# Performance work log

Hardware: AMD Instinct MI355X
Metric: run time of the kernel (lower is better)

Reference implementation:

```python
import jax, jax.numpy as jnp
import numpy as np

N, E, C, D, A, F_, H, RNF = 20000, 200000, 14, 3, 16, 128, 128, 128
CONSTANT = 1.0
LN_EPS = 1e-5


def _pool_matrix(n_channel, dtype):
    ones = np.ones((n_channel, n_channel))
    mats = []
    for i in range(n_channel):
        ws = n_channel - i
        mats.append((np.triu(ones) - np.triu(ones, k=ws)) / ws)
    return jnp.asarray(np.stack(mats), dtype)  # [C, C, C]


def _scatter_mean(src, idx, n):
    s = jax.ops.segment_sum(src, idx, num_segments=n)
    cnt = jax.ops.segment_sum(jnp.ones((src.shape[0],), src.dtype), idx, num_segments=n)
    return s / jnp.maximum(cnt, 1.0).reshape((n,) + (1,) * (src.ndim - 1))


def setup_inputs() -> dict:
    key = jax.random.key(0)
    ks = jax.random.split(key, 24)
    h = jax.random.normal(ks[0], (N, F_), jnp.float32)
    x = jax.random.normal(ks[1], (N, C, D), jnp.float32)
    channel_attr = jax.random.normal(ks[2], (N, C, A), jnp.float32)
    cw = jax.random.uniform(ks[3], (N, C), jnp.float32)
    cw = cw * (jax.random.uniform(ks[4], (N, C)) > 0.3)  # some padded channels
    cw = cw.at[:, 0].set(jax.random.uniform(ks[5], (N,)) + 0.1)  # >=1 valid channel
    row = jax.random.randint(ks[6], (E,), 0, N, dtype=jnp.int32)
    col = jax.random.randint(ks[7], (E,), 0, N, dtype=jnp.int32)

    def lin(k, din, dout):
        return 0.02 * jax.random.normal(k, (din, dout), jnp.float32), jnp.zeros((dout,), jnp.float32)

    rad_w, rad_b = lin(ks[8], A * A, RNF)
    e_w1, e_b1 = lin(ks[9], 2 * F_ + RNF, H)
    e_w2, e_b2 = lin(ks[10], H, H)
    att_w, att_b = lin(ks[11], H, 1)
    c_w1, c_b1 = lin(ks[12], H, H)
    c_w2, c_b2 = lin(ks[13], H, C)
    n_w1, n_b1 = lin(ks[14], F_ + H, H)
    n_w2, n_b2 = lin(ks[15], H, F_)
    ln_g = jnp.ones((F_,), jnp.float32)
    ln_b = jnp.zeros((F_,), jnp.float32)
    return dict(h=h, x=x, channel_attr=channel_attr, channel_weights=cw, row=row, col=col,
                rad_w=rad_w, rad_b=rad_b, e_w1=e_w1, e_b1=e_b1, e_w2=e_w2, e_b2=e_b2,
                att_w=att_w, att_b=att_b, c_w1=c_w1, c_b1=c_b1, c_w2=c_w2, c_b2=c_b2,
                n_w1=n_w1, n_b1=n_b1, n_w2=n_w2, n_b2=n_b2, ln_g=ln_g, ln_b=ln_b)


def reference(h, x, channel_attr, channel_weights, row, col,
              rad_w, rad_b, e_w1, e_b1, e_w2, e_b2, att_w, att_b,
              c_w1, c_b1, c_w2, c_b2, n_w1, n_b1, n_w2, n_b2, ln_g, ln_b):
    silu = jax.nn.silu
    n_nodes = h.shape[0]

    # ---- coord2radial (NUM_SEG = 1) ----
    # pairwise channel distances per edge: [E, C, C]
    coord_msg = jnp.linalg.norm(x[row][:, :, None, :] - x[col][:, None, :, :], axis=-1)
    coord_msg = coord_msg * (channel_weights[row][:, :, None] * channel_weights[col][:, None, :])
    # attr^T @ msg @ attr -> [E, A, A] -> [E, A*A]
    radial = jnp.einsum('eca,ecd,edb->eab', channel_attr[row], coord_msg, channel_attr[col])
    radial = radial.reshape(radial.shape[0], -1)
    radial_norm = jnp.linalg.norm(radial, axis=-1, keepdims=True) + CONSTANT
    radial = (radial @ rad_w + rad_b) / radial_norm

    channel_mask = (channel_weights != 0).astype(x.dtype)  # [N, C]
    channel_sum = jnp.sum(channel_weights != 0, axis=-1).astype(jnp.int32)  # [N]
    pooled_col = (x[col] * channel_mask[col][:, :, None]).sum(1) / channel_sum[col].astype(x.dtype)[:, None]
    coord_diff = x[row] - pooled_col[:, None, :]  # [E, C, 3]

    # ---- edge MLP + attention gate ----
    ef = silu(jnp.concatenate([h[row], h[col], radial], axis=-1) @ e_w1 + e_b1)
    ef = silu(ef @ e_w2 + e_b2)
    ef = ef * jax.nn.sigmoid(ef @ att_w + att_b)  # att_mlp active (hidden_nf == input_nf)

    # ---- RollerPooling on coord_mlp output ----
    cm = silu(ef @ c_w1 + c_b1) @ c_w2 + c_b2  # [E, C]
    pool_mat = _pool_matrix(C, ef.dtype)[channel_sum[row] - 1]  # [E, C, C]
    pooled = jnp.einsum('eij,ej->ei', pool_mat, cm)  # [E, C]
    trans = coord_diff * pooled[:, :, None]  # [E, C, 3]

    x_new = x + _scatter_mean(trans, row, n_nodes)
    agg = _scatter_mean(ef, col, n_nodes)

    nh = silu(jnp.concatenate([h, agg], axis=-1) @ n_w1 + n_b1) @ n_w2 + n_b2
    hr = h + nh
    mu = hr.mean(-1, keepdims=True)
    var = ((hr - mu) ** 2).mean(-1, keepdims=True)
    h_new = (hr - mu) * jax.lax.rsqrt(var + LN_EPS) * ln_g + ln_b
    return h_new, x_new
```

## Files before the change

kernel.cpp:

```cpp
#include <hip/hip_runtime.h>
#include <hip/hip_bf16.h>


#define TE 16
#define TM 64
#define TN 16
#define PAD 36

typedef __attribute__((ext_vector_type(8))) short bf16x8;
typedef __attribute__((ext_vector_type(4))) float f32x4;

__device__ __forceinline__ float siluf(float v) { return v / (1.f + __expf(-v)); }
__device__ __forceinline__ float sigmf(float v) { return 1.f / (1.f + __expf(-v)); }
__device__ __forceinline__ short f2bs(float f) {
  union { __hip_bfloat16 b; short s; } u;
  u.b = __float2bfloat16(f);
  return u.s;
}
__device__ __forceinline__ __hip_bfloat162 mk_bf162(float v0, float v1) {
  __hip_bfloat162 r;
  r.x = __float2bfloat16(v0);
  r.y = __float2bfloat16(v1);
  return r;
}

__global__ __launch_bounds__(256) void k_pack(
    const float* __restrict__ h, const float* __restrict__ x,
    const float* __restrict__ attr, const float* __restrict__ cw,
    const float* __restrict__ rad_w, const float* __restrict__ e_w1,
    const float* __restrict__ e_w2, const float* __restrict__ c_w1,
    const float* __restrict__ n_w1, const float* __restrict__ n_w2,
    const float* __restrict__ c_w2,
    __hip_bfloat16* __restrict__ wz_rad, __hip_bfloat16* __restrict__ wz_e1,
    __hip_bfloat16* __restrict__ wz_e2, __hip_bfloat16* __restrict__ wz_c1,
    __hip_bfloat16* __restrict__ wz_n1, __hip_bfloat16* __restrict__ wz_n2,
    __hip_bfloat16* __restrict__ wz_c2,
    __hip_bfloat16* __restrict__ attrS, __hip_bfloat16* __restrict__ hb,
    float* __restrict__ pooled_x, int* __restrict__ chsum, int Nn) {
  int idx = blockIdx.x * 256 + threadIdx.x;
  if (idx < 165888) {
    int i = idx;
    if (i >= 163840) {
      int base = i - 163840;
      int k = base >> 4, n = base & 15;
      wz_c2[(size_t)(k >> 5) * 512 + n * 32 + (k & 31)] =
          (n < 14) ? __float2bfloat16(c_w2[k * 14 + n]) : __float2bfloat16(0.f);
      return;
    }
    const float* W;
    __hip_bfloat16* O;
    int base;
    if (i < 32768) { W = rad_w; O = wz_rad; base = i; }
    else if (i < 81920) { W = e_w1; O = wz_e1; base = i - 32768; }
    else if (i < 98304) { W = e_w2; O = wz_e2; base = i - 81920; }
    else if (i < 114688) { W = c_w1; O = wz_c1; base = i - 98304; }
    else if (i < 147456) { W = n_w1; O = wz_n1; base = i - 114688; }
    else { W = n_w2; O = wz_n2; base = i - 147456; }
    int k = base >> 7, n = base & 127;
    O[(size_t)((k >> 5) * 128 + n) * 32 + (k & 31)] = __float2bfloat16(W[base]);
    return;
  }
  idx -= 165888;
  int na = Nn * 256, nh = Nn * 128;
  if (idx < na) {
    int n = idx >> 8, r = idx & 255, i2 = r >> 4, a = r & 15;
    float v = 0.f;
    if (i2 < 14) v = attr[(size_t)n * 224 + i2 * 16 + a] * cw[(size_t)n * 14 + i2];
    attrS[(size_t)n * 256 + a * 16 + i2] = __float2bfloat16(v);
    return;
  }
  idx -= na;
  if (idx < nh) {
    hb[idx] = __float2bfloat16(h[idx]);
    return;
  }
  idx -= nh;
  if (idx >= Nn) return;
  int n = idx;
  int cnt = 0;
  float sx = 0.f, sy = 0.f, sz = 0.f;
#pragma unroll
  for (int c = 0; c < 14; c++) {
    float w = cw[n * 14 + c];
    if (w != 0.f) {
      cnt++;
      sx += x[n * 42 + c * 3 + 0];
      sy += x[n * 42 + c * 3 + 1];
      sz += x[n * 42 + c * 3 + 2];
    }
  }
  chsum[n] = cnt;
  float inv = 1.f / (float)(cnt > 0 ? cnt : 1);
  pooled_x[n * 3 + 0] = sx * inv;
  pooled_x[n * 3 + 1] = sy * inv;
  pooled_x[n * 3 + 2] = sz * inv;
}

__global__ __launch_bounds__(256) void k_rad(
    const float* __restrict__ x, const __hip_bfloat16* __restrict__ attrS,
    const int* __restrict__ row, const int* __restrict__ col,
    const __hip_bfloat16* __restrict__ wz_rad, const float* __restrict__ rad_b,
    unsigned* __restrict__ cnt_row, unsigned* __restrict__ cnt_col,
    __hip_bfloat16* __restrict__ radf, int Ee) {
  __shared__ __hip_bfloat16 sW[8][16][PAD];
  __shared__ float s_rn[TE];

  const int t = threadIdx.x;
  const int e0 = blockIdx.x * TE;
  const int ne = min(TE, Ee - e0);

  if (t < ne) {
    atomicAdd(&cnt_row[row[e0 + t]], 1u);
    atomicAdd(&cnt_col[col[e0 + t]], 1u);
  }

  const int lane = t & 63, wave = t >> 6, quad = lane >> 4, mr = lane & 15;
  const int n0 = wave * 32;
  f32x4 zacc = {0.f, 0.f, 0.f, 0.f};
  const bf16x8 zero8 = {0, 0, 0, 0, 0, 0, 0, 0};

  float xr0v[4], xr1v[4], xr2v[4], xc0v[4], xc1v[4], xc2v[4];
  bf16x8 bCv[4], aRv[4];
#pragma unroll
  for (int p = 0; p < 4; p++) {
    const int e = wave * 4 + p;
    const int ge = e0 + min(e, ne - 1);
    const int re = row[ge], ce = col[ge];
    const int mrc = min(mr, 13);
    const float* xp = x + (size_t)re * 42 + mrc * 3;
    xr0v[p] = xp[0]; xr1v[p] = xp[1]; xr2v[p] = xp[2];
    const float* xq = x + (size_t)ce * 42 + mrc * 3;
    xc0v[p] = xq[0]; xc1v[p] = xq[1]; xc2v[p] = xq[2];
    bCv[p] = zero8; aRv[p] = zero8;
    if (quad < 2) {
      bCv[p] = *(const bf16x8*)&attrS[(size_t)ce * 256 + mr * 16 + quad * 8];
      aRv[p] = *(const bf16x8*)&attrS[(size_t)re * 256 + mr * 16 + quad * 8];
    }
  }

#pragma unroll
  for (int p = 0; p < 4; p++) {
    const int e = wave * 4 + p;
    const float xr0 = xr0v[p], xr1 = xr1v[p], xr2 = xr2v[p];
    const float xc0 = xc0v[p], xc1 = xc1v[p], xc2 = xc2v[p];
    bf16x8 aX = zero8, bX = zero8;
    if (quad == 0) {
      aX[0] = f2bs(xc0); aX[1] = f2bs(xc1); aX[2] = f2bs(xc2);
      bX[0] = f2bs(xr0); bX[1] = f2bs(xr1); bX[2] = f2bs(xr2);
    }
    f32x4 G = __builtin_amdgcn_mfma_f32_16x16x32_bf16(aX, bX, zacc, 0, 0, 0);
    const float nr = xr0 * xr0 + xr1 * xr1 + xr2 * xr2;
    const float nc = xc0 * xc0 + xc1 * xc1 + xc2 * xc2;
    float dD[4];
#pragma unroll
    for (int r = 0; r < 4; r++) {
      float ncj = __shfl(nc, quad * 4 + r);
      dD[r] = sqrtf(fmaxf(ncj + nr - 2.f * G[r], 0.f));
    }
    bf16x8 aD;
#pragma unroll
    for (int jj = 0; jj < 8; jj++) {
      const int qs = (quad * 2 + (jj >> 2)) & 3;
      float dv = __shfl(dD[jj & 3], (qs << 4) | mr);
      if (quad >= 2) dv = 0.f;
      aD[jj] = f2bs(dv);
    }
    f32x4 m1 = __builtin_amdgcn_mfma_f32_16x16x32_bf16(aD, bCv[p], zacc, 0, 0, 0);
    bf16x8 bM;
#pragma unroll
    for (int jj = 0; jj < 8; jj++) {
      const int qs = (quad * 2 + (jj >> 2)) & 3;
      float mv = __shfl(m1[jj & 3], (qs << 4) | mr);
      if (quad >= 2) mv = 0.f;
      bM[jj] = f2bs(mv);
    }
    f32x4 rd = __builtin_amdgcn_mfma_f32_16x16x32_bf16(aRv[p], bM, zacc, 0, 0, 0);
    float ss = rd[0] * rd[0] + rd[1] * rd[1] + rd[2] * rd[2] + rd[3] * rd[3];
    ss += __shfl_xor(ss, 32); ss += __shfl_xor(ss, 16); ss += __shfl_xor(ss, 8);
    ss += __shfl_xor(ss, 4);  ss += __shfl_xor(ss, 2);  ss += __shfl_xor(ss, 1);
    if (lane == 0) s_rn[e] = sqrtf(ss) + 1.0f;
#pragma unroll
    for (int r = 0; r < 4; r++) {
      const int aa = quad * 4 + r;
      sW[aa >> 1][e][((aa & 1) << 4) | mr] = __float2bfloat16(rd[r]);
    }
  }
  __syncthreads();

  {
    f32x4 acc0 = zacc, acc1 = zacc;
#pragma unroll
    for (int kb = 0; kb < 8; kb++) {
      bf16x8 a = *(const bf16x8*)&sW[kb][mr][quad * 8];
      const __hip_bfloat16* wp = wz_rad + ((size_t)(kb * 128 + n0 + mr) * 32 + quad * 8);
      bf16x8 b0 = *(const bf16x8*)wp;
      bf16x8 b1 = *(const bf16x8*)(wp + 16 * 32);
      acc0 = __builtin_amdgcn_mfma_f32_16x16x32_bf16(a, b0, acc0, 0, 0, 0);
      acc1 = __builtin_amdgcn_mfma_f32_16x16x32_bf16(a, b1, acc1, 0, 0, 0);
    }
    float bias0 = rad_b[n0 + mr], bias1 = rad_b[n0 + 16 + mr];
#pragma unroll
    for (int r = 0; r < 4; r++) {
      int e = quad * 4 + r;
      if (e < ne) {
        float inv = 1.f / s_rn[e];
        size_t base = (size_t)(e0 + e) * 128;
        radf[base + n0 + mr]      = __float2bfloat16((acc0[r] + bias0) * inv);
        radf[base + n0 + 16 + mr] = __float2bfloat16((acc1[r] + bias1) * inv);
      }
    }
  }
}

__global__ __launch_bounds__(256, 3) void k_mlp(
    const __hip_bfloat16* __restrict__ hb, const __hip_bfloat16* __restrict__ radf,
    const float* __restrict__ x, const float* __restrict__ pooled_x,
    const int* __restrict__ row, const int* __restrict__ col,
    const int* __restrict__ chsum,
    const __hip_bfloat16* __restrict__ wz_e1, const float* __restrict__ e_b1,
    const __hip_bfloat16* __restrict__ wz_e2, const float* __restrict__ e_b2,
    const float* __restrict__ att_w, const float* __restrict__ att_b,
    const __hip_bfloat16* __restrict__ wz_c1, const float* __restrict__ c_b1,
    const __hip_bfloat16* __restrict__ wz_c2, const float* __restrict__ c_b2,
    __hip_bfloat162* __restrict__ x_acc, __hip_bfloat162* __restrict__ agg,
    int Ee) {
  __shared__ __hip_bfloat16 S[12][TM][32];
  __shared__ float s_att[TM];
  __shared__ float s_red[4][TM];
  __shared__ int s_row[TM], s_col[TM], s_cs[TM];
  float* s_cm   = (float*)&S[0][0][0];
  float* s_pool = (float*)&S[1][0][0];

  const int t = threadIdx.x;
  const int e0 = blockIdx.x * TM;
  const int ne = min(TM, Ee - e0);

  if (t < TM) {
    int ge = e0 + min(t, ne - 1);
    int r = row[ge];
    s_row[t] = r;
    s_col[t] = col[ge];
    s_cs[t] = chsum[r];
  }
  __syncthreads();

  {
    const int m = t >> 2, part = t & 3;
    const int pc = ((part ^ ((m >> 1) & 3)) << 3);
    const __hip_bfloat16* hr = hb + (size_t)s_row[m] * 128 + part * 8;
    const __hip_bfloat16* hc = hb + (size_t)s_col[m] * 128 + part * 8;
    const __hip_bfloat16* rf = radf + (size_t)(e0 + min(m, ne - 1)) * 128 + part * 8;
#pragma unroll
    for (int kb = 0; kb < 4; kb++) {
      *(int4*)&S[kb][m][pc]     = *(const int4*)&hr[kb * 32];
      *(int4*)&S[4 + kb][m][pc] = *(const int4*)&hc[kb * 32];
      *(int4*)&S[8 + kb][m][pc] = *(const int4*)&rf[kb * 32];
    }
  }
  __syncthreads();

  const int lane = t & 63, wave = t >> 6, quad = lane >> 4, mr = lane & 15;
  const int n0 = wave * 32;
  const int acol = ((quad ^ ((mr >> 1) & 3)) << 3);
  const f32x4 zacc = {0.f, 0.f, 0.f, 0.f};

  f32x4 s1a0[4], s1a1[4];
#pragma unroll
  for (int mf = 0; mf < 4; mf++) { s1a0[mf] = zacc; s1a1[mf] = zacc; }
#pragma unroll
  for (int kb = 0; kb < 12; kb++) {
    const __hip_bfloat16* wp = wz_e1 + ((size_t)(kb * 128 + n0 + mr) * 32 + quad * 8);
    bf16x8 b0 = *(const bf16x8*)wp;
    bf16x8 b1 = *(const bf16x8*)(wp + 16 * 32);
#pragma unroll
    for (int mf = 0; mf < 4; mf++) {
      bf16x8 a = *(const bf16x8*)&S[kb][mf * 16 + mr][acol];
      s1a0[mf] = __builtin_amdgcn_mfma_f32_16x16x32_bf16(a, b0, s1a0[mf], 0, 0, 0);
      s1a1[mf] = __builtin_amdgcn_mfma_f32_16x16x32_bf16(a, b1, s1a1[mf], 0, 0, 0);
    }
  }
  __syncthreads();
  {
    float bias0 = e_b1[n0 + mr], bias1 = e_b1[n0 + 16 + mr];
#pragma unroll
    for (int mf = 0; mf < 4; mf++)
#pragma unroll
      for (int r = 0; r < 4; r++) {
        int e = mf * 16 + quad * 4 + r;
        int es = (e >> 1) & 3;
        int c0 = (((mr >> 3) ^ es) << 3) | (mr & 7);
        int c1 = (((2 | (mr >> 3)) ^ es) << 3) | (mr & 7);
        S[wave][e][c0] = __float2bfloat16(siluf(s1a0[mf][r] + bias0));
        S[wave][e][c1] = __float2bfloat16(siluf(s1a1[mf][r] + bias1));
      }
  }
  __syncthreads();

  const float aw0 = att_w[n0 + mr], aw1 = att_w[n0 + 16 + mr];
  {
    f32x4 a0[4], a1[4];
#pragma unroll
    for (int mf = 0; mf < 4; mf++) { a0[mf] = zacc; a1[mf] = zacc; }
#pragma unroll
    for (int kb = 0; kb < 4; kb++) {
      const __hip_bfloat16* wp = wz_e2 + ((size_t)(kb * 128 + n0 + mr) * 32 + quad * 8);
      bf16x8 b0 = *(const bf16x8*)wp;
      bf16x8 b1 = *(const bf16x8*)(wp + 16 * 32);
#pragma unroll
      for (int mf = 0; mf < 4; mf++) {
        bf16x8 a = *(const bf16x8*)&S[kb][mf * 16 + mr][acol];
        a0[mf] = __builtin_amdgcn_mfma_f32_16x16x32_bf16(a, b0, a0[mf], 0, 0, 0);
        a1[mf] = __builtin_amdgcn_mfma_f32_16x16x32_bf16(a, b1, a1[mf], 0, 0, 0);
      }
    }
    float bias0 = e_b2[n0 + mr], bias1 = e_b2[n0 + 16 + mr];
    float part[4][4];
#pragma unroll
    for (int mf = 0; mf < 4; mf++)
#pragma unroll
      for (int r = 0; r < 4; r++) {
        int e = mf * 16 + quad * 4 + r;
        int es = (e >> 1) & 3;
        int c0 = (((mr >> 3) ^ es) << 3) | (mr & 7);
        int c1 = (((2 | (mr >> 3)) ^ es) << 3) | (mr & 7);
        float v0 = siluf(a0[mf][r] + bias0);
        float v1 = siluf(a1[mf][r] + bias1);
        S[4 + wave][e][c0] = __float2bfloat16(v0);
        S[4 + wave][e][c1] = __float2bfloat16(v1);
        part[mf][r] = v0 * aw0 + v1 * aw1;
      }
#pragma unroll
    for (int msk = 1; msk < 16; msk <<= 1)
#pragma unroll
      for (int mf = 0; mf < 4; mf++)
#pragma unroll
        for (int r = 0; r < 4; r++) part[mf][r] += __shfl_xor(part[mf][r], msk);
    if (mr == 0) {
#pragma unroll
      for (int mf = 0; mf < 4; mf++)
#pragma unroll
        for (int r = 0; r < 4; r++)
          s_red[wave][mf * 16 + quad * 4 + r] = part[mf][r];
    }
  }
  __syncthreads();
  if (t < TM) {
    float s = s_red[0][t] + s_red[1][t] + s_red[2][t] + s_red[3][t];
    s_att[t] = sigmf(s + att_b[0]);
  }
  __syncthreads();

  {
    f32x4 a0[4], a1[4];
#pragma unroll
    for (int mf = 0; mf < 4; mf++) { a0[mf] = zacc; a1[mf] = zacc; }
#pragma unroll
    for (int kb = 0; kb < 4; kb++) {
      const __hip_bfloat16* wp = wz_c1 + ((size_t)(kb * 128 + n0 + mr) * 32 + quad * 8);
      bf16x8 b0 = *(const bf16x8*)wp;
      bf16x8 b1 = *(const bf16x8*)(wp + 16 * 32);
#pragma unroll
      for (int mf = 0; mf < 4; mf++) {
        bf16x8 a = *(const bf16x8*)&S[4 + kb][mf * 16 + mr][acol];
        a0[mf] = __builtin_amdgcn_mfma_f32_16x16x32_bf16(a, b0, a0[mf], 0, 0, 0);
        a1[mf] = __builtin_amdgcn_mfma_f32_16x16x32_bf16(a, b1, a1[mf], 0, 0, 0);
      }
    }
    float bias0 = c_b1[n0 + mr], bias1 = c_b1[n0 + 16 + mr];
#pragma unroll
    for (int mf = 0; mf < 4; mf++)
#pragma unroll
      for (int r = 0; r < 4; r++) {
        int e = mf * 16 + quad * 4 + r;
        int es = (e >> 1) & 3;
        int c0 = (((mr >> 3) ^ es) << 3) | (mr & 7);
        int c1 = (((2 | (mr >> 3)) ^ es) << 3) | (mr & 7);
        float av = s_att[e];
        S[8 + wave][e][c0] = __float2bfloat16(siluf(av * a0[mf][r] + bias0));
        S[8 + wave][e][c1] = __float2bfloat16(siluf(av * a1[mf][r] + bias1));
      }
  }
  __syncthreads();

  {
    f32x4 acc = zacc;
#pragma unroll
    for (int kb = 0; kb < 4; kb++) {
      bf16x8 a = *(const bf16x8*)&S[8 + kb][wave * 16 + mr][acol];
      bf16x8 b = *(const bf16x8*)(wz_c2 + ((size_t)(kb * 16 + mr) * 32 + quad * 8));
      acc = __builtin_amdgcn_mfma_f32_16x16x32_bf16(a, b, acc, 0, 0, 0);
    }
    if (mr < 14) {
      float bias = c_b2[mr];
#pragma unroll
      for (int r = 0; r < 4; r++)
        s_cm[(wave * 16 + quad * 4 + r) * 14 + mr] = acc[r] + bias;
    }
  }
  __syncthreads();

  for (int i = t; i < TM * 14; i += 256) {
    int e = i / 14, c = i % 14;
    int wsz = 15 - s_cs[e];
    int hi = min(c + wsz, 14);
    float s = 0.f;
    for (int j = c; j < hi; j++) s += s_cm[e * 14 + j];
    s_pool[e * 14 + c] = s / (float)wsz;
  }
  __syncthreads();

  for (int i = t; i < TM * 21; i += 256) {
    int e = i / 21, pr = i % 21;
    if (e < ne) {
      int r0 = pr * 2, r1 = r0 + 1;
      const float* xp = x + (size_t)s_row[e] * 42;
      const float* pc = pooled_x + (size_t)s_col[e] * 3;
      float v0 = (xp[r0] - pc[r0 % 3]) * s_pool[e * 14 + r0 / 3];
      float v1 = (xp[r1] - pc[r1 % 3]) * s_pool[e * 14 + r1 / 3];
      unsafeAtomicAdd(&x_acc[(size_t)s_row[e] * 21 + pr], mk_bf162(v0, v1));
    }
  }
  for (int i = t; i < TM * 64; i += 256) {
    int e = i >> 6, o2 = i & 63;
    if (e < ne) {
      float av = s_att[e];
      int c = (o2 & 15) * 2;
      int pc = (((c >> 3) ^ ((e >> 1) & 3)) << 3) | (c & 7);
      const __hip_bfloat16* wp2 = &S[4 + (o2 >> 4)][e][pc];
      float v0 = __bfloat162float(wp2[0]) * av;
      float v1 = __bfloat162float(wp2[1]) * av;
      unsafeAtomicAdd(&agg[(size_t)s_col[e] * 64 + o2], mk_bf162(v0, v1));
    }
  }
}

__global__ __launch_bounds__(256) void k_node(
    const float* __restrict__ h, const __hip_bfloat162* __restrict__ agg,
    const unsigned* __restrict__ cnt_col,
    const __hip_bfloat16* __restrict__ wz_n1, const float* __restrict__ n_b1,
    const __hip_bfloat16* __restrict__ wz_n2, const float* __restrict__ n_b2,
    const float* __restrict__ ln_g, const float* __restrict__ ln_b,
    const float* __restrict__ x, const __hip_bfloat162* __restrict__ x_acc,
    const unsigned* __restrict__ cnt_row,
    float* __restrict__ out_h, float* __restrict__ out_x, int Nn) {
  __shared__ __hip_bfloat16 sA[8][16][PAD];
  __shared__ __hip_bfloat16 sT[4][16][PAD];
  __shared__ float s_h[TN][128];
  __shared__ float s_o[TN][132];
  const int t = threadIdx.x;
  const int nb0 = blockIdx.x * TN;
  const int nn = min(TN, Nn - nb0);

  for (int i = t; i < TN * 21; i += 256) {
    int n = i / 21, pr = i % 21;
    if (n < nn) {
      int gn = nb0 + n;
      unsigned c = cnt_row[gn];
      float inv = 1.f / (float)(c > 0 ? c : 1);
      float2 xa = __bfloat1622float2(x_acc[(size_t)gn * 21 + pr]);
      size_t gi = (size_t)gn * 42 + pr * 2;
      out_x[gi]     = x[gi] + xa.x * inv;
      out_x[gi + 1] = x[gi + 1] + xa.y * inv;
    }
  }

  for (int i = t; i < TN * 64; i += 256) {
    int m = i >> 6, kp = (i & 63) << 1;
    int kb = kp >> 5, kk = kp & 31;
    int gn = nb0 + min(m, nn - 1);
    const float2 hv = *(const float2*)&h[(size_t)gn * 128 + kp];
    sA[kb][m][kk]     = __float2bfloat16(hv.x);
    sA[kb][m][kk + 1] = __float2bfloat16(hv.y);
    s_h[m][kp]     = hv.x;
    s_h[m][kp + 1] = hv.y;
    unsigned c = cnt_col[gn];
    float inv = 1.f / (float)(c > 0 ? c : 1);
    float2 gv = __bfloat1622float2(agg[(size_t)gn * 64 + (kp >> 1)]);
    sA[4 + kb][m][kk]     = __float2bfloat16(gv.x * inv);
    sA[4 + kb][m][kk + 1] = __float2bfloat16(gv.y * inv);
  }
  __syncthreads();
  const int lane = t & 63, wave = t >> 6, quad = lane >> 4, mr = lane & 15;
  const int n0 = wave * 32;
  f32x4 zacc = {0.f, 0.f, 0.f, 0.f};
  {
    f32x4 acc0 = zacc, acc1 = zacc;
#pragma unroll
    for (int kb = 0; kb < 8; kb++) {
      bf16x8 a = *(const bf16x8*)&sA[kb][mr][quad * 8];
      const __hip_bfloat16* wp = wz_n1 + ((size_t)(kb * 128 + n0 + mr) * 32 + quad * 8);
      bf16x8 b0 = *(const bf16x8*)wp;
      bf16x8 b1 = *(const bf16x8*)(wp + 16 * 32);
      acc0 = __builtin_amdgcn_mfma_f32_16x16x32_bf16(a, b0, acc0, 0, 0, 0);
      acc1 = __builtin_amdgcn_mfma_f32_16x16x32_bf16(a, b1, acc1, 0, 0, 0);
    }
    float bias0 = n_b1[n0 + mr], bias1 = n_b1[n0 + 16 + mr];
#pragma unroll
    for (int r = 0; r < 4; r++) {
      int m = quad * 4 + r;
      sT[wave][m][mr]      = __float2bfloat16(siluf(acc0[r] + bias0));
      sT[wave][m][16 + mr] = __float2bfloat16(siluf(acc1[r] + bias1));
    }
  }
  __syncthreads();
  {
    f32x4 acc0 = zacc, acc1 = zacc;
#pragma unroll
    for (int kb = 0; kb < 4; kb++) {
      bf16x8 a = *(const bf16x8*)&sT[kb][mr][quad * 8];
      const __hip_bfloat16* wp = wz_n2 + ((size_t)(kb * 128 + n0 + mr) * 32 + quad * 8);
      bf16x8 b0 = *(const bf16x8*)wp;
      bf16x8 b1 = *(const bf16x8*)(wp + 16 * 32);
      acc0 = __builtin_amdgcn_mfma_f32_16x16x32_bf16(a, b0, acc0, 0, 0, 0);
      acc1 = __builtin_amdgcn_mfma_f32_16x16x32_bf16(a, b1, acc1, 0, 0, 0);
    }
    float bias0 = n_b2[n0 + mr], bias1 = n_b2[n0 + 16 + mr];
#pragma unroll
    for (int r = 0; r < 4; r++) {
      int m = quad * 4 + r;
      s_o[m][n0 + mr]      = s_h[m][n0 + mr] + acc0[r] + bias0;
      s_o[m][n0 + 16 + mr] = s_h[m][n0 + 16 + mr] + acc1[r] + bias1;
    }
  }
  __syncthreads();
  {
    int n = t >> 4, p = t & 15;
    float v[8];
    float s = 0.f;
#pragma unroll
    for (int j = 0; j < 8; j++) {
      v[j] = s_o[n][p * 8 + j];
      s += v[j];
    }
    s += __shfl_xor(s, 1); s += __shfl_xor(s, 2);
    s += __shfl_xor(s, 4); s += __shfl_xor(s, 8);
    float mu = s * (1.f / 128.f);
    float var = 0.f;
#pragma unroll
    for (int j = 0; j < 8; j++) {
      float d = v[j] - mu;
      var += d * d;
    }
    var += __shfl_xor(var, 1); var += __shfl_xor(var, 2);
    var += __shfl_xor(var, 4); var += __shfl_xor(var, 8);
    float rs = rsqrtf(var * (1.f / 128.f) + 1e-5f);
    if (n < nn) {
      size_t base = (size_t)(nb0 + n) * 128 + p * 8;
#pragma unroll
      for (int j = 0; j < 8; j++)
        out_h[base + j] = (v[j] - mu) * rs * ln_g[p * 8 + j] + ln_b[p * 8 + j];
    }
  }
}

extern "C" void kernel_launch(void* const* d_in, const int* in_sizes, int n_in,
                              void* d_out, int out_size, void* d_ws, size_t ws_size,
                              hipStream_t stream) {
  const float* h     = (const float*)d_in[0];
  const float* x     = (const float*)d_in[1];
  const float* attr  = (const float*)d_in[2];
  const float* cw    = (const float*)d_in[3];
  const int*   row   = (const int*)d_in[4];
  const int*   col   = (const int*)d_in[5];
  const float* rad_w = (const float*)d_in[6];
  const float* rad_b = (const float*)d_in[7];
  const float* e_w1  = (const float*)d_in[8];
  const float* e_b1  = (const float*)d_in[9];
  const float* e_w2  = (const float*)d_in[10];
  const float* e_b2  = (const float*)d_in[11];
  const float* att_w = (const float*)d_in[12];
  const float* att_b = (const float*)d_in[13];
  const float* c_w1  = (const float*)d_in[14];
  const float* c_b1  = (const float*)d_in[15];
  const float* c_w2  = (const float*)d_in[16];
  const float* c_b2  = (const float*)d_in[17];
  const float* n_w1  = (const float*)d_in[18];
  const float* n_b1  = (const float*)d_in[19];
  const float* n_w2  = (const float*)d_in[20];
  const float* n_b2  = (const float*)d_in[21];
  const float* ln_g  = (const float*)d_in[22];
  const float* ln_b  = (const float*)d_in[23];

  const int N = in_sizes[0] / 128;
  const int E = in_sizes[4];

  char* ws = (char*)d_ws;
  size_t off = 0;
  auto alloc = [&](size_t bytes) {
    size_t o = off;
    off += (bytes + 255) & ~(size_t)255;
    return o;
  };
  size_t off_wzr  = alloc(32768 * sizeof(__hip_bfloat16));
  size_t off_wz1  = alloc(49152 * sizeof(__hip_bfloat16));
  size_t off_wz2  = alloc(16384 * sizeof(__hip_bfloat16));
  size_t off_wzc  = alloc(16384 * sizeof(__hip_bfloat16));
  size_t off_wzn1 = alloc(32768 * sizeof(__hip_bfloat16));
  size_t off_wzn2 = alloc(16384 * sizeof(__hip_bfloat16));
  size_t off_wzc2 = alloc(2048 * sizeof(__hip_bfloat16));
  size_t off_atS  = alloc((size_t)N * 256 * sizeof(__hip_bfloat16));
  size_t off_hb   = alloc((size_t)N * 128 * sizeof(__hip_bfloat16));
  size_t off_radf = alloc((size_t)E * 128 * sizeof(__hip_bfloat16));
  size_t off_px   = alloc((size_t)N * 3 * sizeof(float));
  size_t off_cs   = alloc((size_t)N * sizeof(int));
  size_t off_cntr = alloc((size_t)N * sizeof(unsigned));
  size_t off_cntc = alloc((size_t)N * sizeof(unsigned));
  size_t off_xacc = alloc((size_t)N * 21 * sizeof(__hip_bfloat162));
  size_t off_agg  = alloc((size_t)N * 64 * sizeof(__hip_bfloat162));

  __hip_bfloat16* wz_rad = (__hip_bfloat16*)(ws + off_wzr);
  __hip_bfloat16* wz_e1  = (__hip_bfloat16*)(ws + off_wz1);
  __hip_bfloat16* wz_e2  = (__hip_bfloat16*)(ws + off_wz2);
  __hip_bfloat16* wz_c1  = (__hip_bfloat16*)(ws + off_wzc);
  __hip_bfloat16* wz_n1  = (__hip_bfloat16*)(ws + off_wzn1);
  __hip_bfloat16* wz_n2  = (__hip_bfloat16*)(ws + off_wzn2);
  __hip_bfloat16* wz_c2  = (__hip_bfloat16*)(ws + off_wzc2);
  __hip_bfloat16* attrS  = (__hip_bfloat16*)(ws + off_atS);
  __hip_bfloat16* hb     = (__hip_bfloat16*)(ws + off_hb);
  __hip_bfloat16* radf   = (__hip_bfloat16*)(ws + off_radf);
  float* pooled_x   = (float*)(ws + off_px);
  int* chsum        = (int*)(ws + off_cs);
  unsigned* cnt_row = (unsigned*)(ws + off_cntr);
  unsigned* cnt_col = (unsigned*)(ws + off_cntc);
  __hip_bfloat162* x_acc = (__hip_bfloat162*)(ws + off_xacc);
  __hip_bfloat162* agg   = (__hip_bfloat162*)(ws + off_agg);

  (void)hipMemsetAsync(ws + off_cntr, 0, off - off_cntr, stream);

  const int pack_items = 165888 + N * 256 + N * 128 + N;
  k_pack<<<dim3((pack_items + 255) / 256), dim3(256), 0, stream>>>(
      h, x, attr, cw, rad_w, e_w1, e_w2, c_w1, n_w1, n_w2, c_w2,
      wz_rad, wz_e1, wz_e2, wz_c1, wz_n1, wz_n2, wz_c2,
      attrS, hb, pooled_x, chsum, N);
  k_rad<<<dim3((E + TE - 1) / TE), dim3(256), 0, stream>>>(
      x, attrS, row, col, wz_rad, rad_b, cnt_row, cnt_col, radf, E);
  k_mlp<<<dim3((E + TM - 1) / TM), dim3(256), 0, stream>>>(
      hb, radf, x, pooled_x, row, col, chsum,
      wz_e1, e_b1, wz_e2, e_b2, att_w, att_b,
      wz_c1, c_b1, wz_c2, c_b2, x_acc, agg, E);
  k_node<<<dim3((N + TN - 1) / TN), dim3(256), 0, stream>>>(
      h, agg, cnt_col, wz_n1, n_b1, wz_n2, n_b2, ln_g, ln_b,
      x, x_acc, cnt_row, (float*)d_out, (float*)d_out + (size_t)N * 128, N);
}
```

Measured before the change: 386.5 us.

## Fuse radial-feature kernel into edge MLP kernel, dropping the radf buffer

Merges k_rad into the edge MLP kernel. Each 64-edge block now computes its radial features with MFMA, runs the 16x16-per-edge projection over a 64-row tile, and writes the result directly into the swizzled shared tile that the first edge layer consumes. This removes the E x 128 bf16 round trip through global memory and one kernel launch. In exchange the fused kernel has more register and shared-memory pressure, and the radial phase is serialized per block before the MLP.

```diff
diff --git a/kernel.cpp b/kernel.cpp
--- a/kernel.cpp
+++ b/kernel.cpp
@@ -2,7 +2,6 @@
 #include <hip/hip_bf16.h>
 
 
-#define TE 16
 #define TM 64
 #define TN 16
 #define PAD 36
@@ -96,137 +95,24 @@
   pooled_x[n * 3 + 2] = sz * inv;
 }
 
-__global__ __launch_bounds__(256) void k_rad(
-    const float* __restrict__ x, const __hip_bfloat16* __restrict__ attrS,
+__global__ __launch_bounds__(256, 3) void k_mega(
+    const __hip_bfloat16* __restrict__ hb, const float* __restrict__ x,
+    const __hip_bfloat16* __restrict__ attrS,
     const int* __restrict__ row, const int* __restrict__ col,
+    const float* __restrict__ pooled_x, const int* __restrict__ chsum,
     const __hip_bfloat16* __restrict__ wz_rad, const float* __restrict__ rad_b,
-    unsigned* __restrict__ cnt_row, unsigned* __restrict__ cnt_col,
-    __hip_bfloat16* __restrict__ radf, int Ee) {
-  __shared__ __hip_bfloat16 sW[8][16][PAD];
-  __shared__ float s_rn[TE];
-
-  const int t = threadIdx.x;
-  const int e0 = blockIdx.x * TE;
-  const int ne = min(TE, Ee - e0);
-
-  if (t < ne) {
-    atomicAdd(&cnt_row[row[e0 + t]], 1u);
-    atomicAdd(&cnt_col[col[e0 + t]], 1u);
-  }
-
-  const int lane = t & 63, wave = t >> 6, quad = lane >> 4, mr = lane & 15;
-  const int n0 = wave * 32;
-  f32x4 zacc = {0.f, 0.f, 0.f, 0.f};
-  const bf16x8 zero8 = {0, 0, 0, 0, 0, 0, 0, 0};
-
-  float xr0v[4], xr1v[4], xr2v[4], xc0v[4], xc1v[4], xc2v[4];
-  bf16x8 bCv[4], aRv[4];
-#pragma unroll
-  for (int p = 0; p < 4; p++) {
-    const int e = wave * 4 + p;
-    const int ge = e0 + min(e, ne - 1);
-    const int re = row[ge], ce = col[ge];
-    const int mrc = min(mr, 13);
-    const float* xp = x + (size_t)re * 42 + mrc * 3;
-    xr0v[p] = xp[0]; xr1v[p] = xp[1]; xr2v[p] = xp[2];
-    const float* xq = x + (size_t)ce * 42 + mrc * 3;
-    xc0v[p] = xq[0]; xc1v[p] = xq[1]; xc2v[p] = xq[2];
-    bCv[p] = zero8; aRv[p] = zero8;
-    if (quad < 2) {
-      bCv[p] = *(const bf16x8*)&attrS[(size_t)ce * 256 + mr * 16 + quad * 8];
-      aRv[p] = *(const bf16x8*)&attrS[(size_t)re * 256 + mr * 16 + quad * 8];
-    }
-  }
-
-#pragma unroll
-  for (int p = 0; p < 4; p++) {
-    const int e = wave * 4 + p;
-    const float xr0 = xr0v[p], xr1 = xr1v[p], xr2 = xr2v[p];
-    const float xc0 = xc0v[p], xc1 = xc1v[p], xc2 = xc2v[p];
-    bf16x8 aX = zero8, bX = zero8;
-    if (quad == 0) {
-      aX[0] = f2bs(xc0); aX[1] = f2bs(xc1); aX[2] = f2bs(xc2);
-      bX[0] = f2bs(xr0); bX[1] = f2bs(xr1); bX[2] = f2bs(xr2);
-    }
-    f32x4 G = __builtin_amdgcn_mfma_f32_16x16x32_bf16(aX, bX, zacc, 0, 0, 0);
-    const float nr = xr0 * xr0 + xr1 * xr1 + xr2 * xr2;
-    const float nc = xc0 * xc0 + xc1 * xc1 + xc2 * xc2;
-    float dD[4];
-#pragma unroll
-    for (int r = 0; r < 4; r++) {
-      float ncj = __shfl(nc, quad * 4 + r);
-      dD[r] = sqrtf(fmaxf(ncj + nr - 2.f * G[r], 0.f));
-    }
-    bf16x8 aD;
-#pragma unroll
-    for (int jj = 0; jj < 8; jj++) {
-      const int qs = (quad * 2 + (jj >> 2)) & 3;
-      float dv = __shfl(dD[jj & 3], (qs << 4) | mr);
-      if (quad >= 2) dv = 0.f;
-      aD[jj] = f2bs(dv);
-    }
-    f32x4 m1 = __builtin_amdgcn_mfma_f32_16x16x32_bf16(aD, bCv[p], zacc, 0, 0, 0);
-    bf16x8 bM;
-#pragma unroll
-    for (int jj = 0; jj < 8; jj++) {
-      const int qs = (quad * 2 + (jj >> 2)) & 3;
-      float mv = __shfl(m1[jj & 3], (qs << 4) | mr);
-      if (quad >= 2) mv = 0.f;
-      bM[jj] = f2bs(mv);
-    }
-    f32x4 rd = __builtin_amdgcn_mfma_f32_16x16x32_bf16(aRv[p], bM, zacc, 0, 0, 0);
-    float ss = rd[0] * rd[0] + rd[1] * rd[1] + rd[2] * rd[2] + rd[3] * rd[3];
-    ss += __shfl_xor(ss, 32); ss += __shfl_xor(ss, 16); ss += __shfl_xor(ss, 8);
-    ss += __shfl_xor(ss, 4);  ss += __shfl_xor(ss, 2);  ss += __shfl_xor(ss, 1);
-    if (lane == 0) s_rn[e] = sqrtf(ss) + 1.0f;
-#pragma unroll
-    for (int r = 0; r < 4; r++) {
-      const int aa = quad * 4 + r;
-      sW[aa >> 1][e][((aa & 1) << 4) | mr] = __float2bfloat16(rd[r]);
-    }
-  }
-  __syncthreads();
-
-  {
-    f32x4 acc0 = zacc, acc1 = zacc;
-#pragma unroll
-    for (int kb = 0; kb < 8; kb++) {
-      bf16x8 a = *(const bf16x8*)&sW[kb][mr][quad * 8];
-      const __hip_bfloat16* wp = wz_rad + ((size_t)(kb * 128 + n0 + mr) * 32 + quad * 8);
-      bf16x8 b0 = *(const bf16x8*)wp;
-      bf16x8 b1 = *(const bf16x8*)(wp + 16 * 32);
-      acc0 = __builtin_amdgcn_mfma_f32_16x16x32_bf16(a, b0, acc0, 0, 0, 0);
-      acc1 = __builtin_amdgcn_mfma_f32_16x16x32_bf16(a, b1, acc1, 0, 0, 0);
-    }
-    float bias0 = rad_b[n0 + mr], bias1 = rad_b[n0 + 16 + mr];
-#pragma unroll
-    for (int r = 0; r < 4; r++) {
-      int e = quad * 4 + r;
-      if (e < ne) {
-        float inv = 1.f / s_rn[e];
-        size_t base = (size_t)(e0 + e) * 128;
-        radf[base + n0 + mr]      = __float2bfloat16((acc0[r] + bias0) * inv);
-        radf[base + n0 + 16 + mr] = __float2bfloat16((acc1[r] + bias1) * inv);
-      }
-    }
-  }
-}
-
-__global__ __launch_bounds__(256, 3) void k_mlp(
-    const __hip_bfloat16* __restrict__ hb, const __hip_bfloat16* __restrict__ radf,
-    const float* __restrict__ x, const float* __restrict__ pooled_x,
-    const int* __restrict__ row, const int* __restrict__ col,
-    const int* __restrict__ chsum,
     const __hip_bfloat16* __restrict__ wz_e1, const float* __restrict__ e_b1,
     const __hip_bfloat16* __restrict__ wz_e2, const float* __restrict__ e_b2,
     const float* __restrict__ att_w, const float* __restrict__ att_b,
     const __hip_bfloat16* __restrict__ wz_c1, const float* __restrict__ c_b1,
     const __hip_bfloat16* __restrict__ wz_c2, const float* __restrict__ c_b2,
+    unsigned* __restrict__ cnt_row, unsigned* __restrict__ cnt_col,
     __hip_bfloat162* __restrict__ x_acc, __hip_bfloat162* __restrict__ agg,
     int Ee) {
   __shared__ __hip_bfloat16 S[12][TM][32];
   __shared__ float s_att[TM];
   __shared__ float s_red[4][TM];
+  __shared__ float s_rn[TM];
   __shared__ int s_row[TM], s_col[TM], s_cs[TM];
   float* s_cm   = (float*)&S[0][0][0];
   float* s_pool = (float*)&S[1][0][0];
@@ -234,13 +120,126 @@
   const int t = threadIdx.x;
   const int e0 = blockIdx.x * TM;
   const int ne = min(TM, Ee - e0);
+  const int lane = t & 63, wave = t >> 6, quad = lane >> 4, mr = lane & 15;
+  const int n0 = wave * 32;
+  const f32x4 zacc = {0.f, 0.f, 0.f, 0.f};
+  const bf16x8 zero8 = {0, 0, 0, 0, 0, 0, 0, 0};
 
   if (t < TM) {
     int ge = e0 + min(t, ne - 1);
-    int r = row[ge];
+    int r = row[ge], c = col[ge];
     s_row[t] = r;
-    s_col[t] = col[ge];
+    s_col[t] = c;
     s_cs[t] = chsum[r];
+    if (t < ne) {
+      atomicAdd(&cnt_row[r], 1u);
+      atomicAdd(&cnt_col[c], 1u);
+    }
+  }
+
+#pragma unroll 1
+  for (int b = 0; b < 4; b++) {
+    float xr0v[4], xr1v[4], xr2v[4], xc0v[4], xc1v[4], xc2v[4];
+    bf16x8 bCv[4], aRv[4];
+#pragma unroll
+    for (int p = 0; p < 4; p++) {
+      const int e = wave * 16 + b * 4 + p;
+      const int ge = e0 + min(e, ne - 1);
+      const int re = row[ge], ce = col[ge];
+      const int mrc = min(mr, 13);
+      const float* xp = x + (size_t)re * 42 + mrc * 3;
+      xr0v[p] = xp[0]; xr1v[p] = xp[1]; xr2v[p] = xp[2];
+      const float* xq = x + (size_t)ce * 42 + mrc * 3;
+      xc0v[p] = xq[0]; xc1v[p] = xq[1]; xc2v[p] = xq[2];
+      bCv[p] = zero8; aRv[p] = zero8;
+      if (quad < 2) {
+        bCv[p] = *(const bf16x8*)&attrS[(size_t)ce * 256 + mr * 16 + quad * 8];
+        aRv[p] = *(const bf16x8*)&attrS[(size_t)re * 256 + mr * 16 + quad * 8];
+      }
+    }
+#pragma unroll
+    for (int p = 0; p < 4; p++) {
+      const int e = wave * 16 + b * 4 + p;
+      const float xr0 = xr0v[p], xr1 = xr1v[p], xr2 = xr2v[p];
+      const float xc0 = xc0v[p], xc1 = xc1v[p], xc2 = xc2v[p];
+      bf16x8 aX = zero8, bX = zero8;
+      if (quad == 0) {
+        aX[0] = f2bs(xc0); aX[1] = f2bs(xc1); aX[2] = f2bs(xc2);
+        bX[0] = f2bs(xr0); bX[1] = f2bs(xr1); bX[2] = f2bs(xr2);
+      }
+      f32x4 G = __builtin_amdgcn_mfma_f32_16x16x32_bf16(aX, bX, zacc, 0, 0, 0);
+      const float nr = xr0 * xr0 + xr1 * xr1 + xr2 * xr2;
+      const float nc = xc0 * xc0 + xc1 * xc1 + xc2 * xc2;
+      float dD[4];
+#pragma unroll
+      for (int r = 0; r < 4; r++) {
+        float ncj = __shfl(nc, quad * 4 + r);
+        dD[r] = sqrtf(fmaxf(ncj + nr - 2.f * G[r], 0.f));
+      }
+      bf16x8 aD;
+#pragma unroll
+      for (int jj = 0; jj < 8; jj++) {
+        const int qs = (quad * 2 + (jj >> 2)) & 3;
+        float dv = __shfl(dD[jj & 3], (qs << 4) | mr);
+        if (quad >= 2) dv = 0.f;
+        aD[jj] = f2bs(dv);
+      }
+      f32x4 m1 = __builtin_amdgcn_mfma_f32_16x16x32_bf16(aD, bCv[p], zacc, 0, 0, 0);
+      bf16x8 bM;
+#pragma unroll
+      for (int jj = 0; jj < 8; jj++) {
+        const int qs = (quad * 2 + (jj >> 2)) & 3;
+        float mv = __shfl(m1[jj & 3], (qs << 4) | mr);
+        if (quad >= 2) mv = 0.f;
+        bM[jj] = f2bs(mv);
+      }
+      f32x4 rd = __builtin_amdgcn_mfma_f32_16x16x32_bf16(aRv[p], bM, zacc, 0, 0, 0);
+      float ss = rd[0] * rd[0] + rd[1] * rd[1] + rd[2] * rd[2] + rd[3] * rd[3];
+      ss += __shfl_xor(ss, 32); ss += __shfl_xor(ss, 16); ss += __shfl_xor(ss, 8);
+      ss += __shfl_xor(ss, 4);  ss += __shfl_xor(ss, 2);  ss += __shfl_xor(ss, 1);
+      if (lane == 0) s_rn[e] = sqrtf(ss) + 1.0f;
+#pragma unroll
+      for (int r = 0; r < 4; r++) {
+        const int aa = quad * 4 + r;
+        const int c = ((aa & 1) << 4) | mr;
+        const int pcol = (((c >> 3) ^ ((e >> 1) & 3)) << 3) | (c & 7);
+        S[aa >> 1][e][pcol] = __float2bfloat16(rd[r]);
+      }
+    }
+  }
+  __syncthreads();
+
+  const int acol = ((quad ^ ((mr >> 1) & 3)) << 3);
+
+  {
+    f32x4 a0[4], a1[4];
+#pragma unroll
+    for (int mf = 0; mf < 4; mf++) { a0[mf] = zacc; a1[mf] = zacc; }
+#pragma unroll
+    for (int kb = 0; kb < 8; kb++) {
+      const __hip_bfloat16* wp = wz_rad + ((size_t)(kb * 128 + n0 + mr) * 32 + quad * 8);
+      bf16x8 b0 = *(const bf16x8*)wp;
+      bf16x8 b1 = *(const bf16x8*)(wp + 16 * 32);
+#pragma unroll
+      for (int mf = 0; mf < 4; mf++) {
+        bf16x8 a = *(const bf16x8*)&S[kb][mf * 16 + mr][acol];
+        a0[mf] = __builtin_amdgcn_mfma_f32_16x16x32_bf16(a, b0, a0[mf], 0, 0, 0);
+        a1[mf] = __builtin_amdgcn_mfma_f32_16x16x32_bf16(a, b1, a1[mf], 0, 0, 0);
+      }
+    }
+    float rb0 = rad_b[n0 + mr], rb1 = rad_b[n0 + 16 + mr];
+#pragma unroll
+    for (int mf = 0; mf < 4; mf++)
+#pragma unroll
+      for (int r = 0; r < 4; r++) {
+        int e = mf * 16 + quad * 4 + r;
+        int es = (e >> 1) & 3;
+        int c0 = (((mr >> 3) ^ es) << 3) | (mr & 7);
+        int c1 = (((2 | (mr >> 3)) ^ es) << 3) | (mr & 7);
+        float inv = 1.f / s_rn[e];
+        S[8 + wave][e][c0] = __float2bfloat16((a0[mf][r] + rb0) * inv);
+        S[8 + wave][e][c1] = __float2bfloat16((a1[mf][r] + rb1) * inv);
+      }
   }
   __syncthreads();
 
@@ -249,20 +248,13 @@
     const int pc = ((part ^ ((m >> 1) & 3)) << 3);
     const __hip_bfloat16* hr = hb + (size_t)s_row[m] * 128 + part * 8;
     const __hip_bfloat16* hc = hb + (size_t)s_col[m] * 128 + part * 8;
-    const __hip_bfloat16* rf = radf + (size_t)(e0 + min(m, ne - 1)) * 128 + part * 8;
 #pragma unroll
     for (int kb = 0; kb < 4; kb++) {
       *(int4*)&S[kb][m][pc]     = *(const int4*)&hr[kb * 32];
       *(int4*)&S[4 + kb][m][pc] = *(const int4*)&hc[kb * 32];
-      *(int4*)&S[8 + kb][m][pc] = *(const int4*)&rf[kb * 32];
-    }
-  }
-  __syncthreads();
-
-  const int lane = t & 63, wave = t >> 6, quad = lane >> 4, mr = lane & 15;
-  const int n0 = wave * 32;
-  const int acol = ((quad ^ ((mr >> 1) & 3)) << 3);
-  const f32x4 zacc = {0.f, 0.f, 0.f, 0.f};
+    }
+  }
+  __syncthreads();
 
   f32x4 s1a0[4], s1a1[4];
 #pragma unroll
@@ -600,7 +592,6 @@
   size_t off_wzc2 = alloc(2048 * sizeof(__hip_bfloat16));
   size_t off_atS  = alloc((size_t)N * 256 * sizeof(__hip_bfloat16));
   size_t off_hb   = alloc((size_t)N * 128 * sizeof(__hip_bfloat16));
-  size_t off_radf = alloc((size_t)E * 128 * sizeof(__hip_bfloat16));
   size_t off_px   = alloc((size_t)N * 3 * sizeof(float));
   size_t off_cs   = alloc((size_t)N * sizeof(int));
   size_t off_cntr = alloc((size_t)N * sizeof(unsigned));
@@ -617,7 +608,6 @@
   __hip_bfloat16* wz_c2  = (__hip_bfloat16*)(ws + off_wzc2);
   __hip_bfloat16* attrS  = (__hip_bfloat16*)(ws + off_atS);
   __hip_bfloat16* hb     = (__hip_bfloat16*)(ws + off_hb);
-  __hip_bfloat16* radf   = (__hip_bfloat16*)(ws + off_radf);
   float* pooled_x   = (float*)(ws + off_px);
   int* chsum        = (int*)(ws + off_cs);
   unsigned* cnt_row = (unsigned*)(ws + off_cntr);
@@ -632,12 +622,10 @@
       h, x, attr, cw, rad_w, e_w1, e_w2, c_w1, n_w1, n_w2, c_w2,
       wz_rad, wz_e1, wz_e2, wz_c1, wz_n1, wz_n2, wz_c2,
       attrS, hb, pooled_x, chsum, N);
-  k_rad<<<dim3((E + TE - 1) / TE), dim3(256), 0, stream>>>(
-      x, attrS, row, col, wz_rad, rad_b, cnt_row, cnt_col, radf, E);
-  k_mlp<<<dim3((E + TM - 1) / TM), dim3(256), 0, stream>>>(
-      hb, radf, x, pooled_x, row, col, chsum,
-      wz_e1, e_b1, wz_e2, e_b2, att_w, att_b,
-      wz_c1, c_b1, wz_c2, c_b2, x_acc, agg, E);
+  k_mega<<<dim3((E + TM - 1) / TM), dim3(256), 0, stream>>>(
+      hb, x, attrS, row, col, pooled_x, chsum,
+      wz_rad, rad_b, wz_e1, e_b1, wz_e2, e_b2, att_w, att_b,
+      wz_c1, c_b1, wz_c2, c_b2, cnt_row, cnt_col, x_acc, agg, E);
   k_node<<<dim3((N + TN - 1) / TN), dim3(256), 0, stream>>>(
       h, agg, cnt_col, wz_n1, n_b1, wz_n2, n_b2, ln_g, ln_b,
       x, x_acc, cnt_row, (float*)d_out, (float*)d_out + (size_t)N * 128, N);
```

Result: no change. 388.2 us (+0.5%).
